# Kernel optimization log

Hardware: AMD Instinct MI355X
Metric: run time of the kernel (lower is better)

## Reference

```python
import jax, jax.numpy as jnp
import numpy as np

B, T, F, E, H, D, L = 4096, 20, 32, 128, 2, 64, 3
EPS = 1e-5


def setup_inputs() -> dict:
    key = jax.random.key(0)
    ks = jax.random.split(key, 16)
    n = lambda k, s, sc=0.05: jax.random.normal(k, s, jnp.float32) * sc
    return {
        'tokens': jax.random.randint(ks[0], (B, T), 0, 50000),
        'field_ids': jax.random.randint(ks[1], (B, F - 1), 0, 1000),
        'word_emb': n(ks[2], (50000, 300)),
        'W_tok': n(ks[3], (300, E)),
        'field_tables': n(ks[4], (F - 1, 1000, E), E ** -0.5),
        'Wq': n(ks[5], (L, E, H * D)),
        'Wk': n(ks[6], (L, E, H * D)),
        'Wv': n(ks[7], (L, E, H * D)),
        'Wres': n(ks[8], (L, E, H * D)),
        'ln_g': jnp.ones((L, H * D), jnp.float32),
        'ln_b': jnp.zeros((L, H * D), jnp.float32),
        'dnn_W1': n(ks[9], (F * E, 1024)),
        'bn1_g': jnp.ones((1024,), jnp.float32), 'bn1_b': jnp.zeros((1024,), jnp.float32),
        'bn1_m': jnp.zeros((1024,), jnp.float32), 'bn1_v': jnp.ones((1024,), jnp.float32),
        'dnn_W2': n(ks[10], (1024, 512)),
        'bn2_g': jnp.ones((512,), jnp.float32), 'bn2_b': jnp.zeros((512,), jnp.float32),
        'bn2_m': jnp.zeros((512,), jnp.float32), 'bn2_v': jnp.ones((512,), jnp.float32),
        'dnn_W3': n(ks[11], (512, 128)),
        'dnn_b3': jnp.zeros((128,), jnp.float32),
        'W_last': n(ks[12], (F * H * D + 128, 1)),
        'b_last': jnp.zeros((1,), jnp.float32),
    }


def _layer_norm(o, g, b):
    mu = o.mean(-1, keepdims=True)
    var = o.var(-1, keepdims=True)
    return (o - mu) / jnp.sqrt(var + EPS) * g + b


def reference(tokens, field_ids, word_emb, W_tok, field_tables, Wq, Wk, Wv, Wres,
              ln_g, ln_b, dnn_W1, bn1_g, bn1_b, bn1_m, bn1_v, dnn_W2, bn2_g, bn2_b,
              bn2_m, bn2_v, dnn_W3, dnn_b3, W_last, b_last):
    # EmbeddingBag(mean) over tokens, then linear to emb_length
    tok_e = word_emb[tokens].mean(1) @ W_tok                      # [B, E]
    # per-field one-hot embedding lookup
    fld_e = field_tables[jnp.arange(F - 1)[None, :], field_ids]    # [B, F-1, E]
    emb = jnp.concatenate([tok_e[:, None, :], fld_e], 1)          # [B, F, E]

    x = emb
    for l in range(L):
        # split(num_out,-1)+cat(...,0) == reshape to heads
        q = (x @ Wq[l]).reshape(B, F, H, D)
        k = (x @ Wk[l]).reshape(B, F, H, D)
        v = (x @ Wv[l]).reshape(B, F, H, D)
        w = jax.nn.softmax(jnp.einsum('bqhd,bkhd->bhqk', q, k) / jnp.sqrt(jnp.float32(D)), -1)
        o = jnp.einsum('bhqk,bkhd->bqhd', w, v).reshape(B, F, H * D)
        o = jax.nn.relu(o + x @ Wres[l])
        x = _layer_norm(o, ln_g[l], ln_b[l])

    att = x.reshape(B, F * H * D)

    # DNN branch (eval mode: BN uses running stats, dropout off)
    h = emb.reshape(B, F * E)
    h = jax.nn.relu((h @ dnn_W1 - bn1_m) / jnp.sqrt(bn1_v + EPS) * bn1_g + bn1_b)
    h = jax.nn.relu((h @ dnn_W2 - bn2_m) / jnp.sqrt(bn2_v + EPS) * bn2_g + bn2_b)
    h = h @ dnn_W3 + dnn_b3

    out = jnp.concatenate([att, h], 1) @ W_last + b_last          # [B, 1]
    return jax.nn.sigmoid(out)
```

## Files before the change

### kernel.cpp

```cpp
#include <hip/hip_runtime.h>
#include <hip/hip_bf16.h>
#include <cstdint>

#define B_  4096
#define T_  20
#define F_  32
#define E_  128
#define H_  2
#define D_  64
#define L_  3
#define HD_ 128
#define EPS_ 1e-5f

typedef __bf16 bfv8 __attribute__((ext_vector_type(8)));
typedef __bf16 bfv4 __attribute__((ext_vector_type(4)));
typedef float  f32x4 __attribute__((ext_vector_type(4)));

__device__ __forceinline__ f32x4 mfma16(bfv8 a, bfv8 b, f32x4 c) {
    return __builtin_amdgcn_mfma_f32_16x16x32_bf16(a, b, c, 0, 0, 0);
}

__device__ __forceinline__ void gload16(const __bf16* g, __bf16* l) {
    __builtin_amdgcn_global_load_lds(
        (const __attribute__((address_space(1))) void*)(g),
        (__attribute__((address_space(3))) void*)(l),
        16, 0, 0);
}

__device__ void transpose_pack_body(const float* __restrict__ in,
                                    __bf16* __restrict__ out,
                                    int K, int N, int bx, int by)
{
    __shared__ float t[64][65];
    int k0 = bx * 64, n0 = by * 64;
    int r = threadIdx.x >> 4, c = (threadIdx.x & 15) * 4;
    for (int rr = r; rr < 64; rr += 16) {
        float4 v = *(const float4*)&in[(int64_t)(k0 + rr) * N + n0 + c];
        t[rr][c] = v.x; t[rr][c + 1] = v.y; t[rr][c + 2] = v.z; t[rr][c + 3] = v.w;
    }
    __syncthreads();
    for (int rr = r; rr < 64; rr += 16) {
        bfv4 o;
        o[0] = (__bf16)t[c + 0][rr];
        o[1] = (__bf16)t[c + 1][rr];
        o[2] = (__bf16)t[c + 2][rr];
        o[3] = (__bf16)t[c + 3][rr];
        *(bfv4*)&out[(int64_t)(n0 + rr) * K + k0 + c] = o;
    }
}

__global__ __launch_bounds__(256) void pack_all_kernel(
    const float* __restrict__ Wq, const float* __restrict__ Wk,
    const float* __restrict__ Wv, const float* __restrict__ Wres,
    __bf16* __restrict__ pkw,
    const float* __restrict__ dW1, __bf16* __restrict__ W1t,
    const float* __restrict__ dW2, __bf16* __restrict__ W2t,
    const float* __restrict__ dW3, __bf16* __restrict__ W3t)
{
    int id = blockIdx.x;
    if (id < 96) {
        int mi = id >> 3, tile = id & 7;
        int l = mi >> 2, p = mi & 3;
        const float* Wb = (p == 0 ? Wq : p == 1 ? Wk : p == 2 ? Wv : Wres) + l * 16384;
        int tid = threadIdx.x;
        int ks = tid >> 6, lane = tid & 63;
        int l15 = lane & 15, lgg = lane >> 4;
        const float* src = Wb + (ks * 32 + lgg * 8) * HD_ + tile * 16 + l15;
        __bf16* dst = pkw + (int64_t)mi * 16384 + ((tile * 4 + ks) * 64 + lane) * 8;
        #pragma unroll
        for (int t = 0; t < 8; t++) dst[t] = (__bf16)src[t * HD_];
    } else if (id < 1120) {
        int t = id - 96;
        transpose_pack_body(dW1, W1t, 4096, 1024, t & 63, t >> 6);
    } else if (id < 1248) {
        int t = id - 1120;
        transpose_pack_body(dW2, W2t, 1024, 512, t & 15, t >> 4);
    } else {
        int t = id - 1248;
        transpose_pack_body(dW3, W3t, 512, 128, t & 7, t >> 3);
    }
}

__global__ __launch_bounds__(256) void embed2_kernel(
    const int* __restrict__ tokens, const float* __restrict__ word_emb,
    const float* __restrict__ W_tok,
    const int* __restrict__ field_ids, const float* __restrict__ field_tables,
    __bf16* __restrict__ embbf)
{
    if (blockIdx.x < 2048) {
        __shared__ float m[2][304];
        int half = threadIdx.x >> 7, t7 = threadIdx.x & 127;
        int b = blockIdx.x * 2 + half;
        float a0 = 0.f, a1 = 0.f, a2 = 0.f;
        const int* tb = tokens + b * T_;
        for (int t = 0; t < T_; t++) {
            const float* row = word_emb + (int64_t)tb[t] * 300;
            a0 += row[t7];
            a1 += row[t7 + 128];
            if (t7 < 44) a2 += row[t7 + 256];
        }
        m[half][t7]       = a0 * (1.f / T_);
        m[half][t7 + 128] = a1 * (1.f / T_);
        if (t7 < 44) m[half][t7 + 256] = a2 * (1.f / T_);
        __syncthreads();
        float s = 0.f;
        for (int e = 0; e < 300; e++) s = fmaf(m[half][e], W_tok[e * E_ + t7], s);
        embbf[(int64_t)b * (F_ * E_) + t7] = (__bf16)s;
    } else {
        int64_t base = (int64_t)(blockIdx.x - 2048) * 1024 + threadIdx.x;
        #pragma unroll
        for (int u = 0; u < 4; u++) {
            int64_t idx = base + u * 256;
            int c = (int)(idx & 31);
            int64_t tmp = idx >> 5;
            int f = (int)(tmp % 31);
            int b = (int)(tmp / 31);
            int ident = field_ids[b * 31 + f];
            const float4* src = (const float4*)field_tables;
            float4 val = src[(int64_t)(f * 1000 + ident) * 32 + c];
            bfv4 o;
            o[0] = (__bf16)val.x; o[1] = (__bf16)val.y;
            o[2] = (__bf16)val.z; o[3] = (__bf16)val.w;
            *(bfv4*)&embbf[(int64_t)b * 4096 + (1 + f) * 128 + c * 4] = o;
        }
    }
}

__global__ __launch_bounds__(256) void gemm128_bt_bf16_bn(
    const __bf16* __restrict__ A, const __bf16* __restrict__ Bt,
    __bf16* __restrict__ C, int M, int N, int K,
    const float* __restrict__ gp, const float* __restrict__ bp,
    const float* __restrict__ mp, const float* __restrict__ vp)
{
    __shared__ __bf16 As[128 * 64];
    __shared__ __bf16 Bs[128 * 64];
    const int tid = threadIdx.x;
    const int wid = tid >> 6, lane = tid & 63;
    const int l15 = lane & 15, lg = lane >> 4;
    const int wr = wid >> 1, wc = wid & 1;
    const int bm = blockIdx.x, bn = blockIdx.y;

    const int srow = lane >> 3, sp = lane & 7;
    const __bf16* Ag[4]; const __bf16* Bg[4];
    __bf16* Ad[4]; __bf16* Bd[4];
    #pragma unroll
    for (int ga = 0; ga < 4; ga++) {
        int row = wid * 32 + ga * 8 + srow;
        int slot = sp ^ (row & 7);
        Ag[ga] = A  + (int64_t)(bm * 128 + row) * K + slot * 8;
        Bg[ga] = Bt + (int64_t)(bn * 128 + row) * K + slot * 8;
        Ad[ga] = &As[(wid * 32 + ga * 8) * 64];
        Bd[ga] = &Bs[(wid * 32 + ga * 8) * 64];
    }

    int ar[2][4], br[2][4];
    #pragma unroll
    for (int ks = 0; ks < 2; ks++) {
        #pragma unroll
        for (int mi = 0; mi < 4; mi++) {
            int rowa = wr * 64 + mi * 16 + l15;
            ar[ks][mi] = rowa * 64 + (((ks * 4 + lg) ^ (rowa & 7)) * 8);
            int rowb = wc * 64 + mi * 16 + l15;
            br[ks][mi] = rowb * 64 + (((ks * 4 + lg) ^ (rowb & 7)) * 8);
        }
    }

    f32x4 acc[4][4];
    #pragma unroll
    for (int mi = 0; mi < 4; mi++)
        #pragma unroll
        for (int ni = 0; ni < 4; ni++) acc[mi][ni] = (f32x4){0.f, 0.f, 0.f, 0.f};

    for (int k0 = 0; k0 < K; k0 += 64) {
        #pragma unroll
        for (int ga = 0; ga < 4; ga++) gload16(Ag[ga] + k0, Ad[ga]);
        #pragma unroll
        for (int ga = 0; ga < 4; ga++) gload16(Bg[ga] + k0, Bd[ga]);
        __syncthreads();
        #pragma unroll
        for (int ks = 0; ks < 2; ks++) {
            bfv8 af[4], bf[4];
            #pragma unroll
            for (int mi = 0; mi < 4; mi++) af[mi] = *(const bfv8*)&As[ar[ks][mi]];
            #pragma unroll
            for (int ni = 0; ni < 4; ni++) bf[ni] = *(const bfv8*)&Bs[br[ks][ni]];
            #pragma unroll
            for (int mi = 0; mi < 4; mi++)
                #pragma unroll
                for (int ni = 0; ni < 4; ni++)
                    acc[mi][ni] = mfma16(af[mi], bf[ni], acc[mi][ni]);
        }
        __syncthreads();
    }

    float inv[4], sh[4];
    #pragma unroll
    for (int ni = 0; ni < 4; ni++) {
        int col = bn * 128 + wc * 64 + ni * 16 + l15;
        float iv = rsqrtf(vp[col] + EPS_) * gp[col];
        inv[ni] = iv;
        sh[ni] = bp[col] - mp[col] * iv;
    }
    #pragma unroll
    for (int mi = 0; mi < 4; mi++)
        #pragma unroll
        for (int ni = 0; ni < 4; ni++) {
            int col = bn * 128 + wc * 64 + ni * 16 + l15;
            #pragma unroll
            for (int r = 0; r < 4; r++) {
                int row = bm * 128 + wr * 64 + mi * 16 + lg * 4 + r;
                float y = fmaxf(fmaf(acc[mi][ni][r], inv[ni], sh[ni]), 0.f);
                C[(int64_t)row * N + col] = (__bf16)y;
            }
        }
}

template <int OUTBF, int EPI>
__global__ __launch_bounds__(256) void gemm_bt_bf16(
    const __bf16* __restrict__ A, const __bf16* __restrict__ Bt,
    void* __restrict__ Cout, int M, int N, int K,
    const float* __restrict__ gp, const float* __restrict__ bp,
    const float* __restrict__ mp, const float* __restrict__ vp)
{
    __shared__ __bf16 As[128 * 64];
    __shared__ __bf16 Bs[64 * 64];
    const int tid = threadIdx.x;
    const int wid = tid >> 6, lane = tid & 63;
    const int l15 = lane & 15, lg = lane >> 4;
    const int wr = wid >> 1, wc = wid & 1;
    const int bm = blockIdx.x, bn = blockIdx.y;

    const int srow = lane >> 3, sp = lane & 7;
    const __bf16* Ag[4]; const __bf16* Bg[2];
    __bf16* Ad[4]; __bf16* Bd[2];
    #pragma unroll
    for (int ga = 0; ga < 4; ga++) {
        int row = wid * 32 + ga * 8 + srow;
        int slot = sp ^ (row & 7);
        Ag[ga] = A + (int64_t)(bm * 128 + row) * K + slot * 8;
        Ad[ga] = &As[(wid * 32 + ga * 8) * 64];
    }
    #pragma unroll
    for (int gb = 0; gb < 2; gb++) {
        int row = wid * 16 + gb * 8 + srow;
        int slot = sp ^ (row & 7);
        Bg[gb] = Bt + (int64_t)(bn * 64 + row) * K + slot * 8;
        Bd[gb] = &Bs[(wid * 16 + gb * 8) * 64];
    }

    int ar[2][4], br2[2][2];
    #pragma unroll
    for (int ks = 0; ks < 2; ks++) {
        #pragma unroll
        for (int mi = 0; mi < 4; mi++) {
            int row = wr * 64 + mi * 16 + l15;
            ar[ks][mi] = row * 64 + (((ks * 4 + lg) ^ (row & 7)) * 8);
        }
        #pragma unroll
        for (int ni = 0; ni < 2; ni++) {
            int row = wc * 32 + ni * 16 + l15;
            br2[ks][ni] = row * 64 + (((ks * 4 + lg) ^ (row & 7)) * 8);
        }
    }

    f32x4 acc[4][2];
    #pragma unroll
    for (int mi = 0; mi < 4; mi++)
        #pragma unroll
        for (int ni = 0; ni < 2; ni++) acc[mi][ni] = (f32x4){0.f, 0.f, 0.f, 0.f};

    for (int k0 = 0; k0 < K; k0 += 64) {
        #pragma unroll
        for (int ga = 0; ga < 4; ga++) gload16(Ag[ga] + k0, Ad[ga]);
        #pragma unroll
        for (int gb = 0; gb < 2; gb++) gload16(Bg[gb] + k0, Bd[gb]);
        __syncthreads();
        #pragma unroll
        for (int ks = 0; ks < 2; ks++) {
            bfv8 af[4], bf2[2];
            #pragma unroll
            for (int mi = 0; mi < 4; mi++) af[mi] = *(const bfv8*)&As[ar[ks][mi]];
            #pragma unroll
            for (int ni = 0; ni < 2; ni++) bf2[ni] = *(const bfv8*)&Bs[br2[ks][ni]];
            #pragma unroll
            for (int mi = 0; mi < 4; mi++)
                #pragma unroll
                for (int ni = 0; ni < 2; ni++)
                    acc[mi][ni] = mfma16(af[mi], bf2[ni], acc[mi][ni]);
        }
        __syncthreads();
    }

    float inv[2], sh[2];
    #pragma unroll
    for (int ni = 0; ni < 2; ni++) {
        int col = bn * 64 + wc * 32 + ni * 16 + l15;
        if constexpr (EPI == 0) {
            float iv = rsqrtf(vp[col] + EPS_) * gp[col];
            inv[ni] = iv;
            sh[ni] = bp[col] - mp[col] * iv;
        } else {
            inv[ni] = 1.f;
            sh[ni] = bp[col];
        }
    }
    #pragma unroll
    for (int mi = 0; mi < 4; mi++)
        #pragma unroll
        for (int ni = 0; ni < 2; ni++) {
            int col = bn * 64 + wc * 32 + ni * 16 + l15;
            #pragma unroll
            for (int r = 0; r < 4; r++) {
                int row = bm * 128 + wr * 64 + mi * 16 + lg * 4 + r;
                float y = fmaf(acc[mi][ni][r], inv[ni], sh[ni]);
                if constexpr (EPI == 0) y = fmaxf(y, 0.f);
                if constexpr (OUTBF)
                    ((__bf16*)Cout)[(int64_t)row * N + col] = (__bf16)y;
                else
                    ((float*)Cout)[(int64_t)row * N + col] = y;
            }
        }
}

__global__ __launch_bounds__(512, 4) void attn3_head_kernel(
    const __bf16* __restrict__ embbf, const __bf16* __restrict__ pkw,
    const float* __restrict__ lng, const float* __restrict__ lnb,
    const float* __restrict__ h3, const float* __restrict__ Wl,
    const float* __restrict__ bl, float* __restrict__ out)
{
    __shared__ __bf16 smem[8192 * 4 + 4096];
    __shared__ float  part[2][128];
    __bf16* xs  = smem;
    __bf16* qf  = smem + 8192;
    __bf16* kf  = smem + 16384;
    __bf16* vtf = smem + 24576;
    __bf16* pf  = smem + 32768;
    __bf16* wrs = qf;

    const int tid = threadIdx.x;
    const int wid = tid >> 6, lane = tid & 63;
    const int l15 = lane & 15, lg = lane >> 4;
    const int arow = wid >> 2, h = (wid >> 1) & 1, qh = wid & 1;
    const int q = qh * 16 + l15;
    const int half = (lg & 1) * 4;

    {
        const __bf16* src = embbf + (int64_t)blockIdx.x * 8192;
        #pragma unroll
        for (int u = 0; u < 2; u++) {
            int g = u * 512 + tid;
            int ln = g & 63;
            int fld = (((g >> 8) & 1) << 4) + (ln & 15);
            int e0 = ((g >> 6) & 3) * 32 + (ln >> 4) * 8;
            int br = g >> 9;
            bfv8 v = *(const bfv8*)&src[br * 4096 + fld * 128 + e0];
            *(bfv8*)&xs[g * 8] = v;
        }
    }
    __syncthreads();

    float head_partial = 0.f;

    for (int l = 0; l < L_; l++) {
        #pragma unroll 1
        for (int cc = 0; cc < 3; cc++) {
            const int col = wid * 3 + cc;
            const int mat = col >> 3, m = col & 7;
            const __bf16* W = pkw + (l * 4 + mat) * 16384;
            bfv8 wf[4];
            #pragma unroll
            for (int ks = 0; ks < 4; ks++)
                wf[ks] = *(const bfv8*)(W + ((m * 4 + ks) * 64 + lane) * 8);
            f32x4 pc[4];
            #pragma unroll
            for (int i = 0; i < 4; i++) pc[i] = (f32x4){0.f, 0.f, 0.f, 0.f};

            if (mat == 2) {
                #pragma unroll
                for (int i = 0; i < 4; i++) {
                    int gbase = ((i >> 1) * 8 + (i & 1) * 4) * 64;
                    #pragma unroll
                    for (int ks = 0; ks < 4; ks++) {
                        bfv8 xv = *(const bfv8*)&xs[(gbase + ks * 64 + lane) * 8];
                        pc[i] = mfma16(xv, wf[ks], pc[i]);
                    }
                }
            } else {
                #pragma unroll
                for (int i = 0; i < 4; i++) {
                    int gbase = ((i >> 1) * 8 + (i & 1) * 4) * 64;
                    #pragma unroll
                    for (int ks = 0; ks < 4; ks++) {
                        bfv8 xv = *(const bfv8*)&xs[(gbase + ks * 64 + lane) * 8];
                        pc[i] = mfma16(wf[ks], xv, pc[i]);
                    }
                }
            }

            if (mat == 0) {
                const int ln2 = ((((m << 1) + (lg >> 1)) & 3) << 4) + l15;
                #pragma unroll
                for (int i = 0; i < 4; i++) {
                    bfv4 v4;
                    #pragma unroll
                    for (int r = 0; r < 4; r++) v4[r] = (__bf16)(pc[i][r] * 0.125f);
                    int g = ((i >> 1) * 8 + (i & 1) * 4 + (m >> 1)) * 64 + ln2;
                    *(bfv4*)&qf[g * 8 + half] = v4;
                }
            } else if (mat == 1) {
                const int ln2 = ((((m << 1) + (lg >> 1)) & 3) << 4) + l15;
                #pragma unroll
                for (int i = 0; i < 4; i++) {
                    bfv4 v4;
                    #pragma unroll
                    for (int r = 0; r < 4; r++) v4[r] = (__bf16)pc[i][r];
                    int g = ((i >> 1) * 8 + (i & 1) * 4 + (m >> 1)) * 64 + ln2;
                    *(bfv4*)&kf[g * 8 + half] = v4;
                }
            } else {
                #pragma unroll
                for (int i = 0; i < 4; i++) {
                    bfv4 v4;
                    #pragma unroll
                    for (int r = 0; r < 4; r++) v4[r] = (__bf16)pc[i][r];
                    int lnv = ((((i & 1) * 2 + (lg >> 1)) & 3) << 4) + l15;
                    int g = ((i >> 1) * 8 + m) * 64 + lnv;
                    *(bfv4*)&vtf[g * 8 + half] = v4;
                }
            }
        }
        __syncthreads();

        f32x4 sc2[2] = {(f32x4){0.f, 0.f, 0.f, 0.f}, (f32x4){0.f, 0.f, 0.f, 0.f}};
        #pragma unroll
        for (int ksp = 0; ksp < 2; ksp++) {
            int dks = h * 2 + ksp;
            bfv8 qb = *(const bfv8*)&qf[((arow * 8 + qh * 4 + dks) * 64 + lane) * 8];
            #pragma unroll
            for (int km = 0; km < 2; km++) {
                bfv8 kb = *(const bfv8*)&kf[((arow * 8 + km * 4 + dks) * 64 + lane) * 8];
                sc2[km] = mfma16(kb, qb, sc2[km]);
            }
        }
        __syncthreads();

        {
            const __bf16* Wr = pkw + (l * 4 + 3) * 16384;
            #pragma unroll
            for (int c = 0; c < 4; c++) {
                int g = c * 512 + tid;
                gload16(Wr + g * 8, wrs + g * 8);
            }
        }
        float mx = -1e30f;
        #pragma unroll
        for (int km = 0; km < 2; km++)
            #pragma unroll
            for (int r = 0; r < 4; r++) mx = fmaxf(mx, sc2[km][r]);
        mx = fmaxf(mx, __shfl_xor(mx, 16));
        mx = fmaxf(mx, __shfl_xor(mx, 32));
        float pv[2][4];
        float sum = 0.f;
        #pragma unroll
        for (int km = 0; km < 2; km++)
            #pragma unroll
            for (int r = 0; r < 4; r++) {
                float e = __expf(sc2[km][r] - mx);
                pv[km][r] = e; sum += e;
            }
        sum += __shfl_xor(sum, 16);
        sum += __shfl_xor(sum, 32);
        float inv = 1.f / sum;

        __bf16* pw = pf + wid * 512;
        #pragma unroll
        for (int km = 0; km < 2; km++) {
            int ln2 = (((km * 2 + (lg >> 1)) & 3) << 4) + l15;
            bfv4 v4;
            #pragma unroll
            for (int r = 0; r < 4; r++) v4[r] = (__bf16)(pv[km][r] * inv);
            *(bfv4*)&pw[ln2 * 8 + half] = v4;
        }
        bfv8 pb = *(const bfv8*)&pw[lane * 8];
        f32x4 o[4];
        #pragma unroll
        for (int dm = 0; dm < 4; dm++) {
            bfv8 va = *(const bfv8*)&vtf[((arow * 8 + h * 4 + dm) * 64 + lane) * 8];
            o[dm] = mfma16(va, pb, (f32x4){0.f, 0.f, 0.f, 0.f});
        }
        __syncthreads();

        f32x4 macc[4];
        {
            bfv8 xr[4];
            #pragma unroll
            for (int ks = 0; ks < 4; ks++)
                xr[ks] = *(const bfv8*)&xs[((arow * 8 + qh * 4 + ks) * 64 + lane) * 8];
            #pragma unroll
            for (int dm = 0; dm < 4; dm++) {
                macc[dm] = (f32x4){0.f, 0.f, 0.f, 0.f};
                int m = h * 4 + dm;
                #pragma unroll
                for (int ks = 0; ks < 4; ks++) {
                    bfv8 wf = *(const bfv8*)&wrs[((m * 4 + ks) * 64 + lane) * 8];
                    macc[dm] = mfma16(wf, xr[ks], macc[dm]);
                }
            }
        }

        float yv[4][4];
        float s1 = 0.f, s2 = 0.f;
        #pragma unroll
        for (int dm = 0; dm < 4; dm++) {
            #pragma unroll
            for (int r = 0; r < 4; r++) {
                float v = fmaxf(o[dm][r] + macc[dm][r], 0.f);
                yv[dm][r] = v;
                s1 += v; s2 += v * v;
            }
        }
        s1 += __shfl_xor(s1, 16); s1 += __shfl_xor(s1, 32);
        s2 += __shfl_xor(s2, 16); s2 += __shfl_xor(s2, 32);
        if (lg == 0) { part[arow][q * 4 + h * 2] = s1; part[arow][q * 4 + h * 2 + 1] = s2; }
        __syncthreads();

        f32x4 pt = *(const f32x4*)&part[arow][q * 4];
        float mean = (pt[0] + pt[2]) * (1.f / 128.f);
        float var  = (pt[1] + pt[3]) * (1.f / 128.f) - mean * mean;
        float rstd = rsqrtf(var + EPS_);
        const float* lgp = lng + l * HD_;
        const float* lbp = lnb + l * HD_;

        if (l < L_ - 1) {
            #pragma unroll
            for (int dm = 0; dm < 4; dm++) {
                int j = h * 64 + dm * 16 + lg * 4;
                float4 g  = *(const float4*)(lgp + j);
                float4 bb = *(const float4*)(lbp + j);
                bfv4 y;
                y[0] = (__bf16)((yv[dm][0] - mean) * rstd * g.x + bb.x);
                y[1] = (__bf16)((yv[dm][1] - mean) * rstd * g.y + bb.y);
                y[2] = (__bf16)((yv[dm][2] - mean) * rstd * g.z + bb.z);
                y[3] = (__bf16)((yv[dm][3] - mean) * rstd * g.w + bb.w);
                int ks2 = h * 2 + (dm >> 1);
                int ln2 = (((dm * 2 + (lg >> 1)) & 3) << 4) + l15;
                int g2 = (arow * 8 + qh * 4 + ks2) * 64 + ln2;
                *(bfv4*)&xs[g2 * 8 + half] = y;
            }
            __syncthreads();
        } else {
            #pragma unroll
            for (int dm = 0; dm < 4; dm++) {
                int j = h * 64 + dm * 16 + lg * 4;
                float4 g  = *(const float4*)(lgp + j);
                float4 bb = *(const float4*)(lbp + j);
                float4 w  = *(const float4*)(Wl + q * HD_ + j);
                head_partial = fmaf((yv[dm][0] - mean) * rstd * g.x + bb.x, w.x, head_partial);
                head_partial = fmaf((yv[dm][1] - mean) * rstd * g.y + bb.y, w.y, head_partial);
                head_partial = fmaf((yv[dm][2] - mean) * rstd * g.z + bb.z, w.z, head_partial);
                head_partial = fmaf((yv[dm][3] - mean) * rstd * g.w + bb.w, w.w, head_partial);
            }
        }
    }

    float* red = (float*)pf;
    red[tid] = head_partial;
    __syncthreads();
    if ((wid & 3) == 0) {
        int br = wid >> 2;
        int base = br * 256;
        float s = red[base + lane] + red[base + 64 + lane]
                + red[base + 128 + lane] + red[base + 192 + lane];
        int64_t b0 = (int64_t)blockIdx.x * 2 + br;
        s += h3[b0 * 128 + lane]      * Wl[4096 + lane];
        s += h3[b0 * 128 + 64 + lane] * Wl[4096 + 64 + lane];
        #pragma unroll
        for (int off = 32; off; off >>= 1) s += __shfl_down(s, off);
        if (lane == 0) out[b0] = 1.f / (1.f + __expf(-(s + bl[0])));
    }
}

extern "C" void kernel_launch(void* const* d_in, const int* in_sizes, int n_in,
                              void* d_out, int out_size, void* d_ws, size_t ws_size,
                              hipStream_t stream)
{
    const int*   tokens       = (const int*)  d_in[0];
    const int*   field_ids    = (const int*)  d_in[1];
    const float* word_emb     = (const float*)d_in[2];
    const float* W_tok        = (const float*)d_in[3];
    const float* field_tables = (const float*)d_in[4];
    const float* Wq           = (const float*)d_in[5];
    const float* Wk           = (const float*)d_in[6];
    const float* Wv           = (const float*)d_in[7];
    const float* Wres         = (const float*)d_in[8];
    const float* ln_g         = (const float*)d_in[9];
    const float* ln_b         = (const float*)d_in[10];
    const float* dnn_W1       = (const float*)d_in[11];
    const float* bn1_g        = (const float*)d_in[12];
    const float* bn1_b        = (const float*)d_in[13];
    const float* bn1_m        = (const float*)d_in[14];
    const float* bn1_v        = (const float*)d_in[15];
    const float* dnn_W2       = (const float*)d_in[16];
    const float* bn2_g        = (const float*)d_in[17];
    const float* bn2_b        = (const float*)d_in[18];
    const float* bn2_m        = (const float*)d_in[19];
    const float* bn2_v        = (const float*)d_in[20];
    const float* dnn_W3       = (const float*)d_in[21];
    const float* dnn_b3       = (const float*)d_in[22];
    const float* W_last       = (const float*)d_in[23];
    const float* b_last       = (const float*)d_in[24];
    float* out = (float*)d_out;

    const int64_t embN = (int64_t)B_ * F_ * E_;
    __bf16* embbf = (__bf16*)d_ws;
    float*  h3    = (float*)(embbf + embN);
    __bf16* pkw   = (__bf16*)(h3 + (int64_t)B_ * 128);
    __bf16* W1t   = pkw + 12 * 16384;
    __bf16* W2t   = W1t + (int64_t)1024 * 4096;
    __bf16* W3t   = W2t + (int64_t)512 * 1024;
    __bf16* h1bf  = W3t + (int64_t)128 * 512;
    __bf16* h2bf  = h1bf + (int64_t)B_ * 1024;

    pack_all_kernel<<<1264, 256, 0, stream>>>(
        Wq, Wk, Wv, Wres, pkw, dnn_W1, W1t, dnn_W2, W2t, dnn_W3, W3t);

    embed2_kernel<<<6016, 256, 0, stream>>>(
        tokens, word_emb, W_tok, field_ids, field_tables, embbf);

    gemm128_bt_bf16_bn<<<dim3(32, 8), 256, 0, stream>>>(
        embbf, W1t, h1bf, B_, 1024, 4096, bn1_g, bn1_b, bn1_m, bn1_v);
    gemm_bt_bf16<1, 0><<<dim3(32, 8), 256, 0, stream>>>(
        h1bf, W2t, h2bf, B_, 512, 1024, bn2_g, bn2_b, bn2_m, bn2_v);
    gemm_bt_bf16<0, 1><<<dim3(32, 2), 256, 0, stream>>>(
        h2bf, W3t, h3, B_, 128, 512, nullptr, dnn_b3, nullptr, nullptr);

    attn3_head_kernel<<<B_ / 2, 512, 0, stream>>>(
        embbf, pkw, ln_g, ln_b, h3, W_last, b_last, out);
}
```

Before: 237.9 us.

## Load residual weights directly to registers and fuse residual into attention accumulator

The attention kernel no longer stages the per-layer residual projection weights into shared memory via global_load_lds. Each wave now loads its slice straight from global memory into registers. This removes two block-wide barriers per layer, and the residual matmul now runs before the attention-output MFMA, which accumulates into the same registers. The cost is 16 extra bfv8 registers per thread and uncoalesced, redundant global loads of the weight tile across waves, which could raise register pressure at the 512-thread launch bound.

```diff
diff --git a/kernel.cpp b/kernel.cpp
--- a/kernel.cpp
+++ b/kernel.cpp
@@ -335,7 +335,6 @@
     __bf16* kf  = smem + 16384;
     __bf16* vtf = smem + 24576;
     __bf16* pf  = smem + 32768;
-    __bf16* wrs = qf;
 
     const int tid = threadIdx.x;
     const int wid = tid >> 6, lane = tid & 63;
@@ -431,6 +430,16 @@
         }
         __syncthreads();
 
+        const __bf16* Wr = pkw + (l * 4 + 3) * 16384;
+        bfv8 wr0[4], wr1[4], wr2[4], wr3[4];
+        #pragma unroll
+        for (int ks = 0; ks < 4; ks++) {
+            wr0[ks] = *(const bfv8*)(Wr + (((h * 4 + 0) * 4 + ks) * 64 + lane) * 8);
+            wr1[ks] = *(const bfv8*)(Wr + (((h * 4 + 1) * 4 + ks) * 64 + lane) * 8);
+            wr2[ks] = *(const bfv8*)(Wr + (((h * 4 + 2) * 4 + ks) * 64 + lane) * 8);
+            wr3[ks] = *(const bfv8*)(Wr + (((h * 4 + 3) * 4 + ks) * 64 + lane) * 8);
+        }
+
         f32x4 sc2[2] = {(f32x4){0.f, 0.f, 0.f, 0.f}, (f32x4){0.f, 0.f, 0.f, 0.f}};
         #pragma unroll
         for (int ksp = 0; ksp < 2; ksp++) {
@@ -442,16 +451,26 @@
                 sc2[km] = mfma16(kb, qb, sc2[km]);
             }
         }
-        __syncthreads();
-
+
+        f32x4 macc[4];
         {
-            const __bf16* Wr = pkw + (l * 4 + 3) * 16384;
-            #pragma unroll
-            for (int c = 0; c < 4; c++) {
-                int g = c * 512 + tid;
-                gload16(Wr + g * 8, wrs + g * 8);
-            }
-        }
+            bfv8 xr[4];
+            #pragma unroll
+            for (int ks = 0; ks < 4; ks++)
+                xr[ks] = *(const bfv8*)&xs[((arow * 8 + qh * 4 + ks) * 64 + lane) * 8];
+            macc[0] = (f32x4){0.f, 0.f, 0.f, 0.f};
+            macc[1] = (f32x4){0.f, 0.f, 0.f, 0.f};
+            macc[2] = (f32x4){0.f, 0.f, 0.f, 0.f};
+            macc[3] = (f32x4){0.f, 0.f, 0.f, 0.f};
+            #pragma unroll
+            for (int ks = 0; ks < 4; ks++) {
+                macc[0] = mfma16(wr0[ks], xr[ks], macc[0]);
+                macc[1] = mfma16(wr1[ks], xr[ks], macc[1]);
+                macc[2] = mfma16(wr2[ks], xr[ks], macc[2]);
+                macc[3] = mfma16(wr3[ks], xr[ks], macc[3]);
+            }
+        }
+
         float mx = -1e30f;
         #pragma unroll
         for (int km = 0; km < 2; km++)
@@ -482,30 +501,10 @@
             *(bfv4*)&pw[ln2 * 8 + half] = v4;
         }
         bfv8 pb = *(const bfv8*)&pw[lane * 8];
-        f32x4 o[4];
         #pragma unroll
         for (int dm = 0; dm < 4; dm++) {
             bfv8 va = *(const bfv8*)&vtf[((arow * 8 + h * 4 + dm) * 64 + lane) * 8];
-            o[dm] = mfma16(va, pb, (f32x4){0.f, 0.f, 0.f, 0.f});
-        }
-        __syncthreads();
-
-        f32x4 macc[4];
-        {
-            bfv8 xr[4];
-            #pragma unroll
-            for (int ks = 0; ks < 4; ks++)
-                xr[ks] = *(const bfv8*)&xs[((arow * 8 + qh * 4 + ks) * 64 + lane) * 8];
-            #pragma unroll
-            for (int dm = 0; dm < 4; dm++) {
-                macc[dm] = (f32x4){0.f, 0.f, 0.f, 0.f};
-                int m = h * 4 + dm;
-                #pragma unroll
-                for (int ks = 0; ks < 4; ks++) {
-                    bfv8 wf = *(const bfv8*)&wrs[((m * 4 + ks) * 64 + lane) * 8];
-                    macc[dm] = mfma16(wf, xr[ks], macc[dm]);
-                }
-            }
+            macc[dm] = mfma16(va, pb, macc[dm]);
         }
 
         float yv[4][4];
@@ -514,7 +513,7 @@
         for (int dm = 0; dm < 4; dm++) {
             #pragma unroll
             for (int r = 0; r < 4; r++) {
-                float v = fmaxf(o[dm][r] + macc[dm][r], 0.f);
+                float v = fmaxf(macc[dm][r], 0.f);
                 yv[dm][r] = v;
                 s1 += v; s2 += v * v;
             }
```

After: 240.0 us. Within noise of the previous version (+0.9%).
